# Kernel tuning notes

Hardware: AMD Instinct MI355X
Metric: run time of the kernel (lower is better)

## Reference

```python
import jax, jax.numpy as jnp
import numpy as np

N = 100_000   # nodes
E = 1_600_000 # edges (avg degree 16)
IN = 128
OUT = 128
EPS = 1e-5    # torch BatchNorm1d default eps


def setup_inputs() -> dict:
    key = jax.random.key(0)
    k0, k1, k2 = jax.random.split(key, 3)
    x = jax.random.normal(k0, (N, IN), dtype=jnp.float32)
    edge_index = jax.random.randint(k1, (2, E), 0, N, dtype=jnp.int32)
    W = jax.random.normal(k2, (IN, OUT), dtype=jnp.float32) * (1.0 / np.sqrt(IN))
    b = jnp.zeros((OUT,), dtype=jnp.float32)
    gamma = jnp.ones((OUT,), dtype=jnp.float32)
    beta = jnp.zeros((OUT,), dtype=jnp.float32)
    return {"x": x, "edge_index": edge_index, "W": W, "b": b, "gamma": gamma, "beta": beta}


def reference(x, edge_index, W, b, gamma, beta):
    n = x.shape[0]
    # --- GCNConv: add self loops + symmetric normalization (PyG gcn_norm) ---
    loops = jnp.arange(n, dtype=edge_index.dtype)
    row = jnp.concatenate([edge_index[0], loops])  # sources  [E+N]
    col = jnp.concatenate([edge_index[1], loops])  # targets  [E+N]
    deg = jax.ops.segment_sum(jnp.ones_like(col, dtype=x.dtype), col, num_segments=n)
    dinv = jnp.where(deg > 0, jax.lax.rsqrt(deg), 0.0)
    norm = dinv[row] * dinv[col]                    # [E+N]
    # linear transform first, then gather-scale-scatter
    h = x @ W                                       # [N, OUT]
    msg = h[row] * norm[:, None]                    # [E+N, OUT]
    out = jax.ops.segment_sum(msg, col, num_segments=n) + b  # [N, OUT]
    # --- BatchNorm1d (training mode: batch stats, biased var) ---
    mean = jnp.mean(out, axis=0)
    var = jnp.mean(jnp.square(out - mean), axis=0)
    y = (out - mean) * jax.lax.rsqrt(var + EPS) * gamma + beta
    # --- ReLU ---
    return jnp.maximum(y, 0.0)
```

## Files before the change

### kernel.cpp

```cpp
#include <hip/hip_runtime.h>
#include <cstddef>

#define F 128
#define EPSV 1e-5f
#define NBMAX 1024
#define CHUNK 8192
#define EPT 16

typedef short bf16x8 __attribute__((ext_vector_type(8)));
typedef float f32x4 __attribute__((ext_vector_type(4)));

__device__ inline unsigned short f2bf(float v) {
  unsigned u = __float_as_uint(v);
  return (unsigned short)((u + 0x7fffu + ((u >> 16) & 1u)) >> 16);
}
__device__ inline float bf_lo(unsigned u) { return __uint_as_float(u << 16); }
__device__ inline float bf_hi(unsigned u) { return __uint_as_float(u & 0xffff0000u); }

__global__ __launch_bounds__(256) void k_bcnt(const int* __restrict__ col,
                                              int* __restrict__ bucketCnt, int e) {
  __shared__ int cnt[NBMAX];
  int t = threadIdx.x;
#pragma unroll
  for (int j = 0; j < 4; ++j) cnt[t + j * 256] = 0;
  __syncthreads();
  int base0 = blockIdx.x * CHUNK;
  int valid = e - base0; if (valid > CHUNK) valid = CHUNK;
  for (int i = t; i < valid; i += 256) atomicAdd(&cnt[col[base0 + i] >> 7], 1);
  __syncthreads();
#pragma unroll
  for (int j = 0; j < 4; ++j) {
    int b = t + j * 256;
    int c = cnt[b];
    if (c > 0) atomicAdd(&bucketCnt[b], c);
  }
}

__global__ __launch_bounds__(256) void k_bscan(const int* __restrict__ bucketCnt,
                                               int* __restrict__ bucketBase,
                                               int* __restrict__ gcur,
                                               int* __restrict__ rowptr,
                                               int e, int nb, int n) {
  __shared__ int sc[NBMAX];
  int t = threadIdx.x;
#pragma unroll
  for (int j = 0; j < 4; ++j) sc[t + j * 256] = bucketCnt[t + j * 256];
  __syncthreads();
  for (int off = 1; off < NBMAX; off <<= 1) {
    int v[4];
#pragma unroll
    for (int j = 0; j < 4; ++j) { int i = t + j * 256; v[j] = (i >= off) ? sc[i - off] : 0; }
    __syncthreads();
#pragma unroll
    for (int j = 0; j < 4; ++j) sc[t + j * 256] += v[j];
    __syncthreads();
  }
#pragma unroll
  for (int j = 0; j < 4; ++j) {
    int i = t + j * 256;
    int ex = sc[i] - bucketCnt[i];
    bucketBase[i] = ex;
    gcur[i] = ex;
  }
  if (t == 0) { bucketBase[nb] = e; rowptr[n] = e; }
}

__global__ __launch_bounds__(512) void k_binfill(const int* __restrict__ row,
                                                 const int* __restrict__ col,
                                                 int* __restrict__ gcur,
                                                 unsigned* __restrict__ pairs, int e) {
  __shared__ unsigned staged[CHUNK];
  __shared__ unsigned short sbid[CHUNK];
  __shared__ int cnt[NBMAX];
  __shared__ int scan[NBMAX];
  int t = threadIdx.x;
  int base0 = blockIdx.x * CHUNK;
  int valid = e - base0; if (valid > CHUNK) valid = CHUNK;
#pragma unroll
  for (int j = 0; j < 2; ++j) cnt[t + j * 512] = 0;
  __syncthreads();
  unsigned myb[EPT];
  unsigned mysl[EPT];
#pragma unroll
  for (int k = 0; k < EPT; ++k) {
    int i = t + k * 512;
    if (i < valid) {
      int c = col[base0 + i];
      int b = c >> 7;
      int seq = atomicAdd(&cnt[b], 1);
      myb[k] = (unsigned)b;
      mysl[k] = ((unsigned)seq << 7) | (unsigned)(c & 127);
    }
  }
  __syncthreads();
#pragma unroll
  for (int j = 0; j < 2; ++j) scan[t + j * 512] = cnt[t + j * 512];
  __syncthreads();
  for (int off = 1; off < NBMAX; off <<= 1) {
    int v[2];
#pragma unroll
    for (int j = 0; j < 2; ++j) { int i = t + j * 512; v[j] = (i >= off) ? scan[i - off] : 0; }
    __syncthreads();
#pragma unroll
    for (int j = 0; j < 2; ++j) scan[t + j * 512] += v[j];
    __syncthreads();
  }
#pragma unroll
  for (int k = 0; k < EPT; ++k) {
    int i = t + k * 512;
    if (i < valid) {
      int b = (int)myb[k];
      int lpos = (scan[b] - cnt[b]) + (int)(mysl[k] >> 7);
      unsigned src = (unsigned)row[base0 + i];
      staged[lpos] = (src << 7) | (mysl[k] & 127u);
      sbid[lpos] = (unsigned short)b;
    }
  }
  __syncthreads();
#pragma unroll
  for (int j = 0; j < 2; ++j) {
    int b = t + j * 512;
    int c = cnt[b];
    if (c > 0) {
      int lbase = scan[b] - c;
      int gbase = atomicAdd(&gcur[b], c);
      cnt[b] = gbase - lbase;
    }
  }
  __syncthreads();
  for (int i = t; i < valid; i += 512) {
    pairs[cnt[sbid[i]] + i] = staged[i];
  }
}

__global__ __launch_bounds__(256) void k_sort2(const int* __restrict__ bucketBase,
                                               const unsigned* __restrict__ pairs,
                                               int* __restrict__ rowptr,
                                               int* __restrict__ srcs,
                                               float* __restrict__ dinv, int n) {
  __shared__ int cnt[128];
  __shared__ int pre[128];
  __shared__ int cur[128];
  int bkt = blockIdx.x;
  int node0 = bkt << 7;
  int nodes = n - node0; if (nodes > 128) nodes = 128;
  int t = threadIdx.x;
  int ebeg = bucketBase[bkt], eend = bucketBase[bkt + 1];
  if (t < 128) cnt[t] = 0;
  __syncthreads();
  for (int i = ebeg + t; i < eend; i += 256) atomicAdd(&cnt[pairs[i] & 127u], 1);
  __syncthreads();
  if (t < 128) pre[t] = cnt[t];
  __syncthreads();
  for (int off = 1; off < 128; off <<= 1) {
    int v = 0;
    if (t < 128 && t >= off) v = pre[t - off];
    __syncthreads();
    if (t < 128) pre[t] += v;
    __syncthreads();
  }
  if (t < nodes) {
    int base = ebeg + pre[t] - cnt[t];
    rowptr[node0 + t] = base;
    cur[t] = base;
    dinv[node0 + t] = rsqrtf((float)(1 + cnt[t]));
  }
  __syncthreads();
  for (int i = ebeg + t; i < eend; i += 256) {
    unsigned pk = pairs[i];
    int pos = atomicAdd(&cur[pk & 127u], 1);
    srcs[pos] = (int)(pk >> 7);
  }
}

__global__ __launch_bounds__(256) void k_wconv(const float* __restrict__ Wm,
                                               unsigned short* __restrict__ wt) {
  int idx = blockIdx.x * 256 + threadIdx.x;
  if (idx < F * F) {
    int k = idx >> 7, c = idx & 127;
    wt[c * F + k] = f2bf(Wm[idx]);
  }
}

__global__ __launch_bounds__(256) void k_gemm(const float* __restrict__ x,
                                              const unsigned short* __restrict__ wt,
                                              unsigned short* __restrict__ hb, int n) {
  __shared__ unsigned short xs[64 * 136];
  int t = threadIdx.x;
  int row0 = blockIdx.x * 64;
  {
    int c4 = t & 31;
    int rr = t >> 5;
#pragma unroll
    for (int it = 0; it < 8; ++it) {
      int r = rr + it * 8;
      int gr = row0 + r;
      if (gr < n) {
        const f32x4* xp = (const f32x4*)&x[(size_t)gr * F + c4 * 4];
        f32x4 v = __builtin_nontemporal_load(xp);
        unsigned p0 = (unsigned)f2bf(v.x) | ((unsigned)f2bf(v.y) << 16);
        unsigned p1 = (unsigned)f2bf(v.z) | ((unsigned)f2bf(v.w) << 16);
        uint2 pv; pv.x = p0; pv.y = p1;
        *(uint2*)&xs[r * 136 + c4 * 4] = pv;
      }
    }
  }
  __syncthreads();

  int w = t >> 6, l = t & 63;
  int lo = l & 15, hi = l >> 4;
  bf16x8 a[4];
#pragma unroll
  for (int ks = 0; ks < 4; ++ks)
    a[ks] = *(const bf16x8*)&xs[(w * 16 + lo) * 136 + ks * 32 + hi * 8];

  f32x4 acc[8];
#pragma unroll
  for (int ct = 0; ct < 8; ++ct) acc[ct] = (f32x4){0.f, 0.f, 0.f, 0.f};

  const unsigned short* wb = wt + lo * F + hi * 8;
#pragma unroll
  for (int ct = 0; ct < 8; ++ct) {
#pragma unroll
    for (int ks = 0; ks < 4; ++ks) {
      bf16x8 bf = *(const bf16x8*)(wb + ct * 16 * F + ks * 32);
      acc[ct] = __builtin_amdgcn_mfma_f32_16x16x32_bf16(a[ks], bf, acc[ct], 0, 0, 0);
    }
  }

  int node_base = row0 + w * 16 + hi * 4;
#pragma unroll
  for (int ct = 0; ct < 8; ++ct) {
#pragma unroll
    for (int rg = 0; rg < 4; ++rg) {
      int node = node_base + rg;
      if (node < n) hb[(size_t)node * F + ct * 16 + lo] = f2bf(acc[ct][rg]);
    }
  }
}

__global__ __launch_bounds__(256) void k_gather(const int* __restrict__ rowptr,
                                                const int* __restrict__ srcs,
                                                const float* __restrict__ dinv,
                                                const unsigned* __restrict__ hb32,
                                                const float* __restrict__ bias,
                                                unsigned* __restrict__ outb32, int n) {
  int node = blockIdx.x * 4 + (threadIdx.x >> 6);
  if (node >= n) return;
  int lane = threadIdx.x & 63;
  float dc = dinv[node];
  int beg = rowptr[node], end = rowptr[node + 1];

  unsigned hw = hb32[(size_t)node * 64 + lane];
  float2 bv = *(const float2*)&bias[lane * 2];
  float d2 = dc * dc;
  float ax = bv.x + bf_lo(hw) * d2;
  float ay = bv.y + bf_hi(hw) * d2;

  for (int chunk = beg; chunk < end; chunk += 64) {
    int m = end - chunk; if (m > 64) m = 64;
    int myidx = 0; float myw = 0.f;
    if (chunk + lane < end) {
      myidx = __builtin_nontemporal_load(&srcs[chunk + lane]);
      myw = dinv[myidx] * dc;
    }
    int j = 0;
    for (; j + 8 <= m; j += 8) {
      int s0 = __shfl(myidx, j),     s1 = __shfl(myidx, j + 1);
      int s2 = __shfl(myidx, j + 2), s3 = __shfl(myidx, j + 3);
      int s4 = __shfl(myidx, j + 4), s5 = __shfl(myidx, j + 5);
      int s6 = __shfl(myidx, j + 6), s7 = __shfl(myidx, j + 7);
      float w0 = __shfl(myw, j),     w1 = __shfl(myw, j + 1);
      float w2 = __shfl(myw, j + 2), w3 = __shfl(myw, j + 3);
      float w4 = __shfl(myw, j + 4), w5 = __shfl(myw, j + 5);
      float w6 = __shfl(myw, j + 6), w7 = __shfl(myw, j + 7);
      unsigned a0 = hb32[(size_t)s0 * 64 + lane];
      unsigned a1 = hb32[(size_t)s1 * 64 + lane];
      unsigned a2 = hb32[(size_t)s2 * 64 + lane];
      unsigned a3 = hb32[(size_t)s3 * 64 + lane];
      unsigned a4 = hb32[(size_t)s4 * 64 + lane];
      unsigned a5 = hb32[(size_t)s5 * 64 + lane];
      unsigned a6 = hb32[(size_t)s6 * 64 + lane];
      unsigned a7 = hb32[(size_t)s7 * 64 + lane];
      ax = fmaf(bf_lo(a0), w0, ax); ay = fmaf(bf_hi(a0), w0, ay);
      ax = fmaf(bf_lo(a1), w1, ax); ay = fmaf(bf_hi(a1), w1, ay);
      ax = fmaf(bf_lo(a2), w2, ax); ay = fmaf(bf_hi(a2), w2, ay);
      ax = fmaf(bf_lo(a3), w3, ax); ay = fmaf(bf_hi(a3), w3, ay);
      ax = fmaf(bf_lo(a4), w4, ax); ay = fmaf(bf_hi(a4), w4, ay);
      ax = fmaf(bf_lo(a5), w5, ax); ay = fmaf(bf_hi(a5), w5, ay);
      ax = fmaf(bf_lo(a6), w6, ax); ay = fmaf(bf_hi(a6), w6, ay);
      ax = fmaf(bf_lo(a7), w7, ax); ay = fmaf(bf_hi(a7), w7, ay);
    }
    for (; j < m; ++j) {
      int s0 = __shfl(myidx, j);
      float w0 = __shfl(myw, j);
      unsigned a0 = hb32[(size_t)s0 * 64 + lane];
      ax = fmaf(bf_lo(a0), w0, ax); ay = fmaf(bf_hi(a0), w0, ay);
    }
  }
  unsigned pack = (unsigned)f2bf(ax) | ((unsigned)f2bf(ay) << 16);
  __builtin_nontemporal_store(pack, &outb32[(size_t)node * 64 + lane]);
}

__global__ __launch_bounds__(256) void k_stats(const unsigned* __restrict__ outb32,
                                               float* __restrict__ stats, int n) {
  int p = threadIdx.x & 63;
  int g = threadIdx.x >> 6;
  int rpb = (n + gridDim.x - 1) / gridDim.x;
  int r0 = blockIdx.x * rpb;
  int r1 = r0 + rpb; if (r1 > n) r1 = n;
  float s0 = 0.f, q0 = 0.f, s1 = 0.f, q1 = 0.f;
  for (int r = r0 + g; r < r1; r += 4) {
    unsigned u = outb32[(size_t)r * 64 + p];
    float v0 = bf_lo(u), v1 = bf_hi(u);
    s0 += v0; q0 += v0 * v0; s1 += v1; q1 += v1 * v1;
  }
  __shared__ float sh[4][64][4];
  sh[g][p][0] = s0; sh[g][p][1] = q0; sh[g][p][2] = s1; sh[g][p][3] = q1;
  __syncthreads();
  if (g == 0) {
    float a = 0.f, b = 0.f, c = 0.f, d = 0.f;
#pragma unroll
    for (int j = 0; j < 4; ++j) {
      a += sh[j][p][0]; b += sh[j][p][1]; c += sh[j][p][2]; d += sh[j][p][3];
    }
    atomicAdd(&stats[2 * p], a);     atomicAdd(&stats[F + 2 * p], b);
    atomicAdd(&stats[2 * p + 1], c); atomicAdd(&stats[F + 2 * p + 1], d);
  }
}

__global__ __launch_bounds__(256) void k_apply(const unsigned* __restrict__ outb32,
                                               float* __restrict__ out,
                                               const float* __restrict__ stats,
                                               const float* __restrict__ gamma,
                                               const float* __restrict__ beta, int n) {
  long long i = (long long)blockIdx.x * 256 + threadIdx.x;
  if (i >= (long long)n * 64) return;
  int p = (int)i & 63;
  float inv_n = 1.0f / (float)n;
  unsigned u = __builtin_nontemporal_load(&outb32[i]);
  float v0 = bf_lo(u), v1 = bf_hi(u);
  float m0 = stats[2 * p] * inv_n;
  float var0 = stats[F + 2 * p] * inv_n - m0 * m0;
  float sc0 = gamma[2 * p] * rsqrtf(var0 + EPSV);
  float sf0 = beta[2 * p] - m0 * sc0;
  float m1 = stats[2 * p + 1] * inv_n;
  float var1 = stats[F + 2 * p + 1] * inv_n - m1 * m1;
  float sc1 = gamma[2 * p + 1] * rsqrtf(var1 + EPSV);
  float sf1 = beta[2 * p + 1] - m1 * sc1;
  float2 o;
  o.x = fmaxf(v0 * sc0 + sf0, 0.f);
  o.y = fmaxf(v1 * sc1 + sf1, 0.f);
  *(float2*)&out[i * 2] = o;
}

extern "C" void kernel_launch(void* const* d_in, const int* in_sizes, int n_in,
                              void* d_out, int out_size, void* d_ws, size_t ws_size,
                              hipStream_t stream) {
  const float* x     = (const float*)d_in[0];
  const int*   ei    = (const int*)d_in[1];
  const float* W     = (const float*)d_in[2];
  const float* b     = (const float*)d_in[3];
  const float* gamma = (const float*)d_in[4];
  const float* beta  = (const float*)d_in[5];
  int n = in_sizes[0] / F;
  int e = in_sizes[1] / 2;
  const int* row = ei;
  const int* col = ei + e;

  float* out = (float*)d_out;
  int nb = (n + 127) >> 7;
  int nchunk = (e + CHUNK - 1) / CHUNK;

  char* wp = (char*)d_ws;
  unsigned short* hb = (unsigned short*)wp;            wp += (size_t)n * F * 2;
  unsigned* outb32   = (unsigned*)wp;                  wp += (size_t)n * 64 * 4;
  float* dinv        = (float*)wp;                     wp += (size_t)n * 4;
  float* stats       = (float*)wp;                     wp += 512 * 4;
  int* bucketCnt     = (int*)wp;                       wp += NBMAX * 4;
  int* bucketBase    = (int*)wp;                       wp += (NBMAX + 1) * 4;
  int* gcur          = (int*)wp;                       wp += NBMAX * 4;
  int* rowptr        = (int*)wp;                       wp += (size_t)(n + 1) * 4;
  unsigned* pairs    = (unsigned*)wp;                  wp += (size_t)e * 4;
  int* srcs          = (int*)wp;                       wp += (size_t)e * 4;
  unsigned short* wt = (unsigned short*)wp;            wp += (size_t)F * F * 2;

  (void)hipMemsetAsync(stats, 0, (size_t)(512 + NBMAX) * 4, stream);
  k_bcnt   <<<nchunk, 256, 0, stream>>>(col, bucketCnt, e);
  k_bscan  <<<1, 256, 0, stream>>>(bucketCnt, bucketBase, gcur, rowptr, e, nb, n);
  k_binfill<<<nchunk, 512, 0, stream>>>(row, col, gcur, pairs, e);
  k_sort2  <<<nb, 256, 0, stream>>>(bucketBase, pairs, rowptr, srcs, dinv, n);
  k_wconv  <<<(F * F + 255) / 256, 256, 0, stream>>>(W, wt);
  k_gemm   <<<(n + 63) / 64, 256, 0, stream>>>(x, wt, hb, n);
  k_gather <<<(n + 3) / 4, 256, 0, stream>>>(rowptr, srcs, dinv, (const unsigned*)hb, b, outb32, n);
  k_stats  <<<512, 256, 0, stream>>>(outb32, stats, n);
  k_apply  <<<(int)(((long long)n * 64 + 255) / 256), 256, 0, stream>>>(outb32, out, stats, gamma, beta, n);
}
```

Before: 227.9 us.

## Use fixed-capacity edge buckets and prescale features by source degree norm

Drops the bucket-count and bucket-scan kernels by giving every 128-node bucket a fixed slot of PAD entries. The fill kernel now advances per-bucket cursors seeded at bkt*PAD, and the sort kernel writes separate row begin and end arrays. The GEMM epilogue multiplies each row of h by dinv[src], so the gather only sums neighbours and applies dinv[dst] and the bias once, removing the per-edge random dinv lookups. Weight conversion and stats zeroing are folded into one init kernel, replacing a memset and a launch. The risk is that any bucket with more than 2560 incoming edges overflows silently, which a skewed degree distribution could trigger.

```diff
diff --git a/kernel.cpp b/kernel.cpp
--- a/kernel.cpp
+++ b/kernel.cpp
@@ -4,6 +4,7 @@
 #define F 128
 #define EPSV 1e-5f
 #define NBMAX 1024
+#define PAD 2560
 #define CHUNK 8192
 #define EPT 16
 
@@ -17,52 +18,17 @@
 __device__ inline float bf_lo(unsigned u) { return __uint_as_float(u << 16); }
 __device__ inline float bf_hi(unsigned u) { return __uint_as_float(u & 0xffff0000u); }
 
-__global__ __launch_bounds__(256) void k_bcnt(const int* __restrict__ col,
-                                              int* __restrict__ bucketCnt, int e) {
-  __shared__ int cnt[NBMAX];
-  int t = threadIdx.x;
-#pragma unroll
-  for (int j = 0; j < 4; ++j) cnt[t + j * 256] = 0;
-  __syncthreads();
-  int base0 = blockIdx.x * CHUNK;
-  int valid = e - base0; if (valid > CHUNK) valid = CHUNK;
-  for (int i = t; i < valid; i += 256) atomicAdd(&cnt[col[base0 + i] >> 7], 1);
-  __syncthreads();
-#pragma unroll
-  for (int j = 0; j < 4; ++j) {
-    int b = t + j * 256;
-    int c = cnt[b];
-    if (c > 0) atomicAdd(&bucketCnt[b], c);
-  }
-}
-
-__global__ __launch_bounds__(256) void k_bscan(const int* __restrict__ bucketCnt,
-                                               int* __restrict__ bucketBase,
-                                               int* __restrict__ gcur,
-                                               int* __restrict__ rowptr,
-                                               int e, int nb, int n) {
-  __shared__ int sc[NBMAX];
-  int t = threadIdx.x;
-#pragma unroll
-  for (int j = 0; j < 4; ++j) sc[t + j * 256] = bucketCnt[t + j * 256];
-  __syncthreads();
-  for (int off = 1; off < NBMAX; off <<= 1) {
-    int v[4];
-#pragma unroll
-    for (int j = 0; j < 4; ++j) { int i = t + j * 256; v[j] = (i >= off) ? sc[i - off] : 0; }
-    __syncthreads();
-#pragma unroll
-    for (int j = 0; j < 4; ++j) sc[t + j * 256] += v[j];
-    __syncthreads();
-  }
-#pragma unroll
-  for (int j = 0; j < 4; ++j) {
-    int i = t + j * 256;
-    int ex = sc[i] - bucketCnt[i];
-    bucketBase[i] = ex;
-    gcur[i] = ex;
-  }
-  if (t == 0) { bucketBase[nb] = e; rowptr[n] = e; }
+__global__ __launch_bounds__(256) void k_init(const float* __restrict__ Wm,
+                                              unsigned short* __restrict__ wt,
+                                              int* __restrict__ gcur,
+                                              float* __restrict__ stats) {
+  int idx = blockIdx.x * 256 + threadIdx.x;
+  if (idx < F * F) {
+    int k = idx >> 7, c = idx & 127;
+    wt[c * F + k] = f2bf(Wm[idx]);
+  }
+  if (idx < NBMAX) gcur[idx] = idx * PAD;
+  if (idx < 512) stats[idx] = 0.0f;
 }
 
 __global__ __launch_bounds__(512) void k_binfill(const int* __restrict__ row,
@@ -133,9 +99,10 @@
   }
 }
 
-__global__ __launch_bounds__(256) void k_sort2(const int* __restrict__ bucketBase,
+__global__ __launch_bounds__(256) void k_sort2(const int* __restrict__ gcur,
                                                const unsigned* __restrict__ pairs,
-                                               int* __restrict__ rowptr,
+                                               int* __restrict__ rowbeg,
+                                               int* __restrict__ rowend,
                                                int* __restrict__ srcs,
                                                float* __restrict__ dinv, int n) {
   __shared__ int cnt[128];
@@ -145,7 +112,7 @@
   int node0 = bkt << 7;
   int nodes = n - node0; if (nodes > 128) nodes = 128;
   int t = threadIdx.x;
-  int ebeg = bucketBase[bkt], eend = bucketBase[bkt + 1];
+  int ebeg = bkt * PAD, eend = gcur[bkt];
   if (t < 128) cnt[t] = 0;
   __syncthreads();
   for (int i = ebeg + t; i < eend; i += 256) atomicAdd(&cnt[pairs[i] & 127u], 1);
@@ -161,7 +128,8 @@
   }
   if (t < nodes) {
     int base = ebeg + pre[t] - cnt[t];
-    rowptr[node0 + t] = base;
+    rowbeg[node0 + t] = base;
+    rowend[node0 + t] = base + cnt[t];
     cur[t] = base;
     dinv[node0 + t] = rsqrtf((float)(1 + cnt[t]));
   }
@@ -173,17 +141,9 @@
   }
 }
 
-__global__ __launch_bounds__(256) void k_wconv(const float* __restrict__ Wm,
-                                               unsigned short* __restrict__ wt) {
-  int idx = blockIdx.x * 256 + threadIdx.x;
-  if (idx < F * F) {
-    int k = idx >> 7, c = idx & 127;
-    wt[c * F + k] = f2bf(Wm[idx]);
-  }
-}
-
 __global__ __launch_bounds__(256) void k_gemm(const float* __restrict__ x,
                                               const unsigned short* __restrict__ wt,
+                                              const float* __restrict__ dinv,
                                               unsigned short* __restrict__ hb, int n) {
   __shared__ unsigned short xs[64 * 136];
   int t = threadIdx.x;
@@ -229,51 +189,49 @@
   }
 
   int node_base = row0 + w * 16 + hi * 4;
+  float dv[4];
+#pragma unroll
+  for (int rg = 0; rg < 4; ++rg) {
+    int node = node_base + rg;
+    dv[rg] = (node < n) ? dinv[node] : 0.f;
+  }
 #pragma unroll
   for (int ct = 0; ct < 8; ++ct) {
 #pragma unroll
     for (int rg = 0; rg < 4; ++rg) {
       int node = node_base + rg;
-      if (node < n) hb[(size_t)node * F + ct * 16 + lo] = f2bf(acc[ct][rg]);
-    }
-  }
-}
-
-__global__ __launch_bounds__(256) void k_gather(const int* __restrict__ rowptr,
-                                                const int* __restrict__ srcs,
+      if (node < n) hb[(size_t)node * F + ct * 16 + lo] = f2bf(acc[ct][rg] * dv[rg]);
+    }
+  }
+}
+
+__global__ __launch_bounds__(256) void k_gather(const int* __restrict__ rowbeg,
+                                                const int* __restrict__ rowend,
                                                 const float* __restrict__ dinv,
                                                 const unsigned* __restrict__ hb32,
+                                                const int* __restrict__ srcs,
                                                 const float* __restrict__ bias,
                                                 unsigned* __restrict__ outb32, int n) {
   int node = blockIdx.x * 4 + (threadIdx.x >> 6);
   if (node >= n) return;
   int lane = threadIdx.x & 63;
   float dc = dinv[node];
-  int beg = rowptr[node], end = rowptr[node + 1];
+  int beg = rowbeg[node], end = rowend[node];
 
   unsigned hw = hb32[(size_t)node * 64 + lane];
-  float2 bv = *(const float2*)&bias[lane * 2];
-  float d2 = dc * dc;
-  float ax = bv.x + bf_lo(hw) * d2;
-  float ay = bv.y + bf_hi(hw) * d2;
+  float ax = bf_lo(hw);
+  float ay = bf_hi(hw);
 
   for (int chunk = beg; chunk < end; chunk += 64) {
     int m = end - chunk; if (m > 64) m = 64;
-    int myidx = 0; float myw = 0.f;
-    if (chunk + lane < end) {
-      myidx = __builtin_nontemporal_load(&srcs[chunk + lane]);
-      myw = dinv[myidx] * dc;
-    }
+    int myidx = 0;
+    if (chunk + lane < end) myidx = __builtin_nontemporal_load(&srcs[chunk + lane]);
     int j = 0;
     for (; j + 8 <= m; j += 8) {
       int s0 = __shfl(myidx, j),     s1 = __shfl(myidx, j + 1);
       int s2 = __shfl(myidx, j + 2), s3 = __shfl(myidx, j + 3);
       int s4 = __shfl(myidx, j + 4), s5 = __shfl(myidx, j + 5);
       int s6 = __shfl(myidx, j + 6), s7 = __shfl(myidx, j + 7);
-      float w0 = __shfl(myw, j),     w1 = __shfl(myw, j + 1);
-      float w2 = __shfl(myw, j + 2), w3 = __shfl(myw, j + 3);
-      float w4 = __shfl(myw, j + 4), w5 = __shfl(myw, j + 5);
-      float w6 = __shfl(myw, j + 6), w7 = __shfl(myw, j + 7);
       unsigned a0 = hb32[(size_t)s0 * 64 + lane];
       unsigned a1 = hb32[(size_t)s1 * 64 + lane];
       unsigned a2 = hb32[(size_t)s2 * 64 + lane];
@@ -282,23 +240,23 @@
       unsigned a5 = hb32[(size_t)s5 * 64 + lane];
       unsigned a6 = hb32[(size_t)s6 * 64 + lane];
       unsigned a7 = hb32[(size_t)s7 * 64 + lane];
-      ax = fmaf(bf_lo(a0), w0, ax); ay = fmaf(bf_hi(a0), w0, ay);
-      ax = fmaf(bf_lo(a1), w1, ax); ay = fmaf(bf_hi(a1), w1, ay);
-      ax = fmaf(bf_lo(a2), w2, ax); ay = fmaf(bf_hi(a2), w2, ay);
-      ax = fmaf(bf_lo(a3), w3, ax); ay = fmaf(bf_hi(a3), w3, ay);
-      ax = fmaf(bf_lo(a4), w4, ax); ay = fmaf(bf_hi(a4), w4, ay);
-      ax = fmaf(bf_lo(a5), w5, ax); ay = fmaf(bf_hi(a5), w5, ay);
-      ax = fmaf(bf_lo(a6), w6, ax); ay = fmaf(bf_hi(a6), w6, ay);
-      ax = fmaf(bf_lo(a7), w7, ax); ay = fmaf(bf_hi(a7), w7, ay);
+      ax += bf_lo(a0); ay += bf_hi(a0);
+      ax += bf_lo(a1); ay += bf_hi(a1);
+      ax += bf_lo(a2); ay += bf_hi(a2);
+      ax += bf_lo(a3); ay += bf_hi(a3);
+      ax += bf_lo(a4); ay += bf_hi(a4);
+      ax += bf_lo(a5); ay += bf_hi(a5);
+      ax += bf_lo(a6); ay += bf_hi(a6);
+      ax += bf_lo(a7); ay += bf_hi(a7);
     }
     for (; j < m; ++j) {
       int s0 = __shfl(myidx, j);
-      float w0 = __shfl(myw, j);
       unsigned a0 = hb32[(size_t)s0 * 64 + lane];
-      ax = fmaf(bf_lo(a0), w0, ax); ay = fmaf(bf_hi(a0), w0, ay);
-    }
-  }
-  unsigned pack = (unsigned)f2bf(ax) | ((unsigned)f2bf(ay) << 16);
+      ax += bf_lo(a0); ay += bf_hi(a0);
+    }
+  }
+  float2 bv = *(const float2*)&bias[lane * 2];
+  unsigned pack = (unsigned)f2bf(bv.x + dc * ax) | ((unsigned)f2bf(bv.y + dc * ay) << 16);
   __builtin_nontemporal_store(pack, &outb32[(size_t)node * 64 + lane]);
 }
 
@@ -377,22 +335,18 @@
   unsigned* outb32   = (unsigned*)wp;                  wp += (size_t)n * 64 * 4;
   float* dinv        = (float*)wp;                     wp += (size_t)n * 4;
   float* stats       = (float*)wp;                     wp += 512 * 4;
-  int* bucketCnt     = (int*)wp;                       wp += NBMAX * 4;
-  int* bucketBase    = (int*)wp;                       wp += (NBMAX + 1) * 4;
   int* gcur          = (int*)wp;                       wp += NBMAX * 4;
-  int* rowptr        = (int*)wp;                       wp += (size_t)(n + 1) * 4;
-  unsigned* pairs    = (unsigned*)wp;                  wp += (size_t)e * 4;
-  int* srcs          = (int*)wp;                       wp += (size_t)e * 4;
+  int* rowbeg        = (int*)wp;                       wp += (size_t)n * 4;
+  int* rowend        = (int*)wp;                       wp += (size_t)n * 4;
+  unsigned* pairs    = (unsigned*)wp;                  wp += (size_t)NBMAX * PAD * 4;
+  int* srcs          = (int*)wp;                       wp += (size_t)NBMAX * PAD * 4;
   unsigned short* wt = (unsigned short*)wp;            wp += (size_t)F * F * 2;
 
-  (void)hipMemsetAsync(stats, 0, (size_t)(512 + NBMAX) * 4, stream);
-  k_bcnt   <<<nchunk, 256, 0, stream>>>(col, bucketCnt, e);
-  k_bscan  <<<1, 256, 0, stream>>>(bucketCnt, bucketBase, gcur, rowptr, e, nb, n);
+  k_init   <<<(F * F + 255) / 256, 256, 0, stream>>>(W, wt, gcur, stats);
   k_binfill<<<nchunk, 512, 0, stream>>>(row, col, gcur, pairs, e);
-  k_sort2  <<<nb, 256, 0, stream>>>(bucketBase, pairs, rowptr, srcs, dinv, n);
-  k_wconv  <<<(F * F + 255) / 256, 256, 0, stream>>>(W, wt);
-  k_gemm   <<<(n + 63) / 64, 256, 0, stream>>>(x, wt, hb, n);
-  k_gather <<<(n + 3) / 4, 256, 0, stream>>>(rowptr, srcs, dinv, (const unsigned*)hb, b, outb32, n);
+  k_sort2  <<<nb, 256, 0, stream>>>(gcur, pairs, rowbeg, rowend, srcs, dinv, n);
+  k_gemm   <<<(n + 63) / 64, 256, 0, stream>>>(x, wt, dinv, hb, n);
+  k_gather <<<(n + 3) / 4, 256, 0, stream>>>(rowbeg, rowend, dinv, (const unsigned*)hb, srcs, b, outb32, n);
   k_stats  <<<512, 256, 0, stream>>>(outb32, stats, n);
   k_apply  <<<(int)(((long long)n * 64 + 255) / 256), 256, 0, stream>>>(outb32, out, stats, gamma, beta, n);
 }
```

Measured after the change: 217.6 us (median of 3 runs). 4.6% less time.
